# Kernel optimization log

Hardware: AMD Instinct MI355X
Metric: run time of the kernel (lower is better)

The kernel has to match this reference:

```python
import jax, jax.numpy as jnp
import numpy as np

IRREPS = [(32, 0), (16, 1), (8, 2)]          # (multiplicity, l)
DIMS = [m * (2 * l + 1) for m, l in IRREPS]  # [32, 48, 40]
OFF = np.concatenate([[0], np.cumsum(DIMS)]).astype(int)
FEAT = int(OFF[-1])                          # 120
H = 4                                        # num_heads
EPS = 1e-5
N_NODES = 50000
N_EDGES = 800000


def split(x):
    # split last axis into per-irrep blocks [..., mul, 2l+1]
    return [x[..., OFF[i]:OFF[i + 1]].reshape(x.shape[:-1] + (m, 2 * l + 1))
            for i, (m, l) in enumerate(IRREPS)]


def merge(blocks, lead):
    return jnp.concatenate([b.reshape(lead + (-1,)) for b in blocks], axis=-1)


def o3_linear(x, Ws):
    # e3nn o3.Linear: mixes multiplicities within each irrep type, 1/sqrt(fan_in) norm
    bs = split(x)
    out = [jnp.einsum('...im,io->...om', b, W) / np.sqrt(m)
           for b, W, (m, l) in zip(bs, Ws, IRREPS)]
    return merge(out, x.shape[:-1])


def norm_act(x):
    # e3nn nn.NormActivation with sigmoid: y = sigmoid(|x|) * x / |x| per irrep
    out = []
    for b in split(x):
        n = jnp.sqrt(jnp.sum(b * b, axis=-1, keepdims=True) + EPS * EPS)
        out.append(jax.nn.sigmoid(n) * b / n)
    return merge(out, x.shape[:-1])


def tp_dot(q, k, Wd):
    # FullyConnectedTensorProduct(q_ir, k_ir, 'Hx0e'), component normalization:
    # per-edge weighted inner products between matching irreps -> [E, H]
    fan = sum(m * m * (2 * l + 1) for m, l in IRREPS)
    out = 0.0
    for qb, kb, W, (m, l) in zip(split(q), split(k), Wd, IRREPS):
        out = out + jnp.einsum('eim,ejm,ijh->eh', qb, kb, W) / np.sqrt(2 * l + 1)
    return out / np.sqrt(fan)


def setup_inputs() -> dict:
    key = jax.random.key(0)
    ks = jax.random.split(key, 16)
    inp = {"node_features": jax.random.normal(ks[0], (N_NODES, FEAT), jnp.float32)}
    i = 1
    for name in ("Wq", "Wk", "Wv"):
        for j, (m, l) in enumerate(IRREPS):
            inp[f"{name}{j}"] = jax.random.normal(ks[i], (m, m), jnp.float32); i += 1
    for j, (m, l) in enumerate(IRREPS):
        inp[f"Wd{j}"] = jax.random.normal(ks[i], (m, m, H), jnp.float32); i += 1
    inp["edge_dst"] = jax.random.randint(ks[i], (N_EDGES,), 0, N_NODES); i += 1
    inp["edge_src"] = jax.random.randint(ks[i], (N_EDGES,), 0, N_NODES)
    return inp


def reference(node_features, Wq0, Wq1, Wq2, Wk0, Wk1, Wk2, Wv0, Wv1, Wv2,
              Wd0, Wd1, Wd2, edge_dst, edge_src):
    N = node_features.shape[0]
    q = norm_act(o3_linear(node_features, [Wq0, Wq1, Wq2]))              # [N, F]
    k = norm_act(o3_linear(node_features[edge_src], [Wk0, Wk1, Wk2]))    # [E, F]
    v_node = norm_act(o3_linear(node_features, [Wv0, Wv1, Wv2]))         # [N, F]
    v = v_node[edge_src]                                                 # [E, F]
    exp = jnp.exp(tp_dot(q[edge_dst], k, [Wd0, Wd1, Wd2]))               # [E, H]
    exp = jnp.mean(exp, axis=1, keepdims=True)                           # [E, 1]
    z = jax.ops.segment_sum(exp, edge_dst, num_segments=N)               # [N, 1]
    z = jnp.where(z == 0, 1.0, z)
    alpha = exp / z[edge_dst]                                            # [E, 1]
    f_out = jax.ops.segment_sum(jnp.sqrt(jax.nn.relu(alpha)) * v,
                                edge_dst, num_segments=N)                # [N, F]
    return f_out + v_node
```

## Files before the change

### kernel.cpp

```cpp
#include <hip/hip_runtime.h>
#include <math.h>

#define FEAT 120
#define HCNT 4

typedef unsigned short ushort_t;
typedef unsigned int uint_t;
typedef __attribute__((ext_vector_type(8))) short short8;
typedef __attribute__((ext_vector_type(4))) float floatx4;

__device__ __forceinline__ float nact_scale(float sumsq) {
    float n = sqrtf(sumsq + 1e-10f);
    float sig = 1.0f / (1.0f + expf(-n));
    return sig / n;
}

__device__ __forceinline__ ushort_t bf16r(float f) {
    uint_t u = __float_as_uint(f);
    u += 0x7fff + ((u >> 16) & 1);
    return (ushort_t)(u >> 16);
}

#define INV_S32 0.17677669529663687f
#define INV_S16 0.25f
#define INV_S8  0.35355339059327373f
#define S_IR0 0.02175970668223486f
#define S_IR1 0.012562972567021898f
#define S_IR2 0.009731317442393031f


__global__ __launch_bounds__(256) void zero_int_kernel(int* __restrict__ p, int n) {
    int i = blockIdx.x * 256 + threadIdx.x;
    if (i < n) p[i] = 0;
}

__global__ __launch_bounds__(256) void hist_kernel(const int* __restrict__ dst,
                                                   int* __restrict__ cnt, int E) {
    int e = blockIdx.x * 256 + threadIdx.x;
    if (e < E) atomicAdd(&cnt[dst[e]], 1);
}

__global__ __launch_bounds__(256) void scan_block_kernel(const int* __restrict__ cnt,
                                                         int* __restrict__ excl,
                                                         int* __restrict__ bsum, int n) {
    __shared__ int s[256];
    int t = threadIdx.x;
    int i = blockIdx.x * 256 + t;
    int v = (i < n) ? cnt[i] : 0;
    s[t] = v;
    __syncthreads();
    for (int off = 1; off < 256; off <<= 1) {
        int add = (t >= off) ? s[t - off] : 0;
        __syncthreads();
        s[t] += add;
        __syncthreads();
    }
    if (i < n) excl[i] = s[t] - v;
    if (t == 255) bsum[blockIdx.x] = s[255];
}

__global__ __launch_bounds__(256) void scan_sums_kernel(int* __restrict__ bsum, int nb) {
    __shared__ int s[256];
    int t = threadIdx.x;
    int v = (t < nb) ? bsum[t] : 0;
    s[t] = v;
    __syncthreads();
    for (int off = 1; off < 256; off <<= 1) {
        int add = (t >= off) ? s[t - off] : 0;
        __syncthreads();
        s[t] += add;
        __syncthreads();
    }
    if (t < nb) bsum[t] = s[t] - v;
}

__global__ __launch_bounds__(256) void add_offsets_kernel(int* __restrict__ offsets,
                                                          const int* __restrict__ bsum,
                                                          int* __restrict__ cursor,
                                                          int n, int E) {
    int i = blockIdx.x * 256 + threadIdx.x;
    if (i < n) {
        int off = offsets[i] + bsum[i >> 8];
        offsets[i] = off;
        cursor[i] = off;
    }
    if (i == 0) offsets[n] = E;
}

__global__ __launch_bounds__(256) void scatter_kernel(const int* __restrict__ dst,
                                                      const int* __restrict__ src,
                                                      int* __restrict__ cursor,
                                                      int* __restrict__ ssrc, int E) {
    int e = blockIdx.x * 256 + threadIdx.x;
    if (e < E) {
        int pos = atomicAdd(&cursor[dst[e]], 1);
        ssrc[pos] = src[e];
    }
}


__global__ __launch_bounds__(256) void node_qkv_kernel(
    const float* __restrict__ x,
    const float* __restrict__ Wq0, const float* __restrict__ Wq1, const float* __restrict__ Wq2,
    const float* __restrict__ Wk0, const float* __restrict__ Wk1, const float* __restrict__ Wk2,
    const float* __restrict__ Wv0, const float* __restrict__ Wv1, const float* __restrict__ Wv2,
    float* __restrict__ qnode, ushort_t* __restrict__ kb, ushort_t* __restrict__ vb,
    float* __restrict__ out, int N)
{
    __shared__ float sWq0[1024], sWq1[256], sWq2[64];
    __shared__ float sWk0[1024], sWk1[256], sWk2[64];
    __shared__ float sWv0[1024], sWv1[256], sWv2[64];

    int t = threadIdx.x;
    for (int i = t; i < 1024; i += 256) { sWq0[i] = Wq0[i]; sWk0[i] = Wk0[i]; sWv0[i] = Wv0[i]; }
    if (t < 256) { sWq1[t] = Wq1[t]; sWk1[t] = Wk1[t]; sWv1[t] = Wv1[t]; }
    if (t < 64)  { sWq2[t] = Wq2[t]; sWk2[t] = Wk2[t]; sWv2[t] = Wv2[t]; }
    __syncthreads();

    int lane = t & 63, wid = t >> 6;
    int ngrp = (N + 3) >> 2;
    for (int grp = blockIdx.x; grp < ngrp; grp += gridDim.x) {
        int node = __builtin_amdgcn_readfirstlane(grp * 4 + wid);
        if (node >= N) continue;
        const float* xr = x + (size_t)node * FEAT;
        float* qr = qnode + (size_t)node * FEAT;
        ushort_t* kr = kb + (size_t)node * 128;
        ushort_t* vr = vb + (size_t)node * 128;
        float* orow = out + (size_t)node * FEAT;
        if (lane < 32) {
            int o = lane;
            float q = 0, k = 0, v = 0;
            #pragma unroll 8
            for (int i = 0; i < 32; i++) {
                float xi = xr[i];
                q = fmaf(xi, sWq0[i * 32 + o], q);
                k = fmaf(xi, sWk0[i * 32 + o], k);
                v = fmaf(xi, sWv0[i * 32 + o], v);
            }
            q *= INV_S32; k *= INV_S32; v *= INV_S32;
            q *= nact_scale(q * q);
            k *= nact_scale(k * k);
            v *= nact_scale(v * v);
            qr[o] = q; kr[o] = bf16r(k); vr[o] = bf16r(v); orow[o] = v;
        } else if (lane < 48) {
            int o = lane - 32;
            float q[3] = {0,0,0}, k[3] = {0,0,0}, v[3] = {0,0,0};
            for (int i = 0; i < 16; i++) {
                float wq = sWq1[i * 16 + o], wk = sWk1[i * 16 + o], wv = sWv1[i * 16 + o];
                #pragma unroll
                for (int c = 0; c < 3; c++) {
                    float xi = xr[32 + i * 3 + c];
                    q[c] = fmaf(xi, wq, q[c]);
                    k[c] = fmaf(xi, wk, k[c]);
                    v[c] = fmaf(xi, wv, v[c]);
                }
            }
            float nq = 0, nk = 0, nv = 0;
            #pragma unroll
            for (int c = 0; c < 3; c++) {
                q[c] *= INV_S16; k[c] *= INV_S16; v[c] *= INV_S16;
                nq += q[c]*q[c]; nk += k[c]*k[c]; nv += v[c]*v[c];
            }
            float sq = nact_scale(nq), sk = nact_scale(nk), sv = nact_scale(nv);
            #pragma unroll
            for (int c = 0; c < 3; c++) {
                int f = 32 + o * 3 + c;
                float vv = v[c]*sv;
                qr[f] = q[c]*sq; kr[f] = bf16r(k[c]*sk); vr[f] = bf16r(vv); orow[f] = vv;
            }
        } else if (lane < 56) {
            int o = lane - 48;
            float q[5] = {0,0,0,0,0}, k[5] = {0,0,0,0,0}, v[5] = {0,0,0,0,0};
            for (int i = 0; i < 8; i++) {
                float wq = sWq2[i * 8 + o], wk = sWk2[i * 8 + o], wv = sWv2[i * 8 + o];
                #pragma unroll
                for (int c = 0; c < 5; c++) {
                    float xi = xr[80 + i * 5 + c];
                    q[c] = fmaf(xi, wq, q[c]);
                    k[c] = fmaf(xi, wk, k[c]);
                    v[c] = fmaf(xi, wv, v[c]);
                }
            }
            float nq = 0, nk = 0, nv = 0;
            #pragma unroll
            for (int c = 0; c < 5; c++) {
                q[c] *= INV_S8; k[c] *= INV_S8; v[c] *= INV_S8;
                nq += q[c]*q[c]; nk += k[c]*k[c]; nv += v[c]*v[c];
            }
            float sq = nact_scale(nq), sk = nact_scale(nk), sv = nact_scale(nv);
            #pragma unroll
            for (int c = 0; c < 5; c++) {
                int f = 80 + o * 5 + c;
                float vv = v[c]*sv;
                qr[f] = q[c]*sq; kr[f] = bf16r(k[c]*sk); vr[f] = bf16r(vv); orow[f] = vv;
            }
        } else {
            int p = 120 + (lane - 56);
            kr[p] = 0; vr[p] = 0;
        }
    }
}


__global__ __launch_bounds__(256) void node_tq_kernel(
    const float* __restrict__ qnode,
    const float* __restrict__ Wd0, const float* __restrict__ Wd1, const float* __restrict__ Wd2,
    ushort_t* __restrict__ tqb, int N)
{
    __shared__ float4 sWd0[1024];
    __shared__ float4 sWd1[256];
    __shared__ float4 sWd2[64];
    __shared__ float qs[4][FEAT];

    int t = threadIdx.x;
    for (int i = t; i < 1024; i += 256) sWd0[i] = ((const float4*)Wd0)[i];
    if (t < 256) sWd1[t] = ((const float4*)Wd1)[t];
    if (t < 64)  sWd2[t] = ((const float4*)Wd2)[t];
    __syncthreads();

    int lane = t & 63, wid = t >> 6;
    int ngrp = (N + 3) >> 2;
    for (int grp = blockIdx.x; grp < ngrp; grp += gridDim.x) {
        int node = __builtin_amdgcn_readfirstlane(grp * 4 + wid);
        if (node >= N) continue;
        const float* qr = qnode + (size_t)node * FEAT;
        qs[wid][lane] = qr[lane];
        if (lane < FEAT - 64) qs[wid][64 + lane] = qr[64 + lane];
        __builtin_amdgcn_wave_barrier();

        ushort_t* tr = tqb + (size_t)node * 512;
        if (lane < 32) {
            int j = lane;
            float a0 = 0, a1 = 0, a2 = 0, a3 = 0;
            #pragma unroll 8
            for (int i = 0; i < 32; i++) {
                float qi = qs[wid][i];
                float4 w = sWd0[i * 32 + j];
                a0 = fmaf(qi, w.x, a0); a1 = fmaf(qi, w.y, a1);
                a2 = fmaf(qi, w.z, a2); a3 = fmaf(qi, w.w, a3);
            }
            tr[0 * 128 + j] = bf16r(a0 * S_IR0);
            tr[1 * 128 + j] = bf16r(a1 * S_IR0);
            tr[2 * 128 + j] = bf16r(a2 * S_IR0);
            tr[3 * 128 + j] = bf16r(a3 * S_IR0);
        } else if (lane < 48) {
            int j = lane - 32;
            float a[4][3] = {};
            for (int i = 0; i < 16; i++) {
                float4 w = sWd1[i * 16 + j];
                #pragma unroll
                for (int c = 0; c < 3; c++) {
                    float qi = qs[wid][32 + i * 3 + c];
                    a[0][c] = fmaf(qi, w.x, a[0][c]);
                    a[1][c] = fmaf(qi, w.y, a[1][c]);
                    a[2][c] = fmaf(qi, w.z, a[2][c]);
                    a[3][c] = fmaf(qi, w.w, a[3][c]);
                }
            }
            #pragma unroll
            for (int h = 0; h < 4; h++)
                #pragma unroll
                for (int c = 0; c < 3; c++)
                    tr[h * 128 + 32 + j * 3 + c] = bf16r(a[h][c] * S_IR1);
        } else if (lane < 56) {
            int j = lane - 48;
            float a[4][5] = {};
            for (int i = 0; i < 8; i++) {
                float4 w = sWd2[i * 8 + j];
                #pragma unroll
                for (int c = 0; c < 5; c++) {
                    float qi = qs[wid][80 + i * 5 + c];
                    a[0][c] = fmaf(qi, w.x, a[0][c]);
                    a[1][c] = fmaf(qi, w.y, a[1][c]);
                    a[2][c] = fmaf(qi, w.z, a[2][c]);
                    a[3][c] = fmaf(qi, w.w, a[3][c]);
                }
            }
            #pragma unroll
            for (int h = 0; h < 4; h++)
                #pragma unroll
                for (int c = 0; c < 5; c++)
                    tr[h * 128 + 80 + j * 5 + c] = bf16r(a[h][c] * S_IR2);
        } else {
            int r = lane - 56;
            #pragma unroll
            for (int h = 0; h < 4; h++) tr[h * 128 + 120 + r] = 0;
        }
        __builtin_amdgcn_wave_barrier();
    }
}


__global__ __launch_bounds__(256) void edge_mfma_kernel(
    const ushort_t* __restrict__ tqb, const ushort_t* __restrict__ kb,
    const ushort_t* __restrict__ vb,
    const int* __restrict__ offsets, const int* __restrict__ ssrc,
    float* __restrict__ out, int N)
{
    int lane = threadIdx.x & 63, wid = threadIdx.x >> 6;
    int node = blockIdx.x * 4 + wid;
    if (node >= N) return;
    node = __builtin_amdgcn_readfirstlane(node);
    int m = lane & 15, quad = lane >> 4;

    short8 afr[4];
    if (m < HCNT) {
        const short8* ap = (const short8*)(tqb + (size_t)node * 512 + m * 128 + quad * 8);
        #pragma unroll
        for (int b = 0; b < 4; b++) afr[b] = ap[b * 4];
    } else {
        #pragma unroll
        for (int b = 0; b < 4; b++) afr[b] = (short8){0,0,0,0,0,0,0,0};
    }

    int beg = offsets[node], end = offsets[node + 1];
    float zpart = 0.0f, accx = 0.0f, accy = 0.0f;
    const uint_t* vrow = (const uint_t*)vb;

    for (int tb = beg; tb < end; tb += 16) {
        int rem = end - tb; if (rem > 16) rem = 16;
        int idx = tb + (m < rem ? m : rem - 1);
        int src = ssrc[idx];
        const short8* bp = (const short8*)(kb + (size_t)src * 128 + quad * 8);
        short8 b0 = bp[0], b1 = bp[4], b2 = bp[8], b3 = bp[12];
        floatx4 C = {0.0f, 0.0f, 0.0f, 0.0f};
        C = __builtin_amdgcn_mfma_f32_16x16x32_bf16(afr[0], b0, C, 0, 0, 0);
        C = __builtin_amdgcn_mfma_f32_16x16x32_bf16(afr[1], b1, C, 0, 0, 0);
        C = __builtin_amdgcn_mfma_f32_16x16x32_bf16(afr[2], b2, C, 0, 0, 0);
        C = __builtin_amdgcn_mfma_f32_16x16x32_bf16(afr[3], b3, C, 0, 0, 0);

        float w = 0.0f;
        if (quad == 0 && m < rem) {
            float ex = 0.25f * (__expf(C[0]) + __expf(C[1]) + __expf(C[2]) + __expf(C[3]));
            zpart += ex;
            w = sqrtf(ex);
        }

        if (rem == 16) {
            #pragma unroll
            for (int e0 = 0; e0 < 16; e0 += 8) {
                float we[8]; int se[8]; uint_t vp[8];
                #pragma unroll
                for (int j = 0; j < 8; j++) {
                    we[j] = __shfl(w, e0 + j, 64);
                    se[j] = __shfl(src, e0 + j, 64);
                }
                #pragma unroll
                for (int j = 0; j < 8; j++) vp[j] = vrow[(size_t)se[j] * 64 + lane];
                #pragma unroll
                for (int j = 0; j < 8; j++) {
                    accx = fmaf(we[j], __uint_as_float(vp[j] << 16), accx);
                    accy = fmaf(we[j], __uint_as_float(vp[j] & 0xffff0000u), accy);
                }
            }
        } else {
            for (int e = 0; e < rem; e++) {
                float we = __shfl(w, e, 64);
                int   se = __shfl(src, e, 64);
                uint_t vp = vrow[(size_t)se * 64 + lane];
                accx = fmaf(we, __uint_as_float(vp << 16), accx);
                accy = fmaf(we, __uint_as_float(vp & 0xffff0000u), accy);
            }
        }
    }

    zpart += __shfl_xor(zpart, 1, 64);
    zpart += __shfl_xor(zpart, 2, 64);
    zpart += __shfl_xor(zpart, 4, 64);
    zpart += __shfl_xor(zpart, 8, 64);
    float zsum = __shfl(zpart, 0, 64);
    float scale = (zsum > 0.0f) ? rsqrtf(zsum) : 0.0f;

    if (lane < 60) {
        float2* op = (float2*)(out + (size_t)node * FEAT) + lane;
        float2 o = *op;
        o.x = fmaf(accx, scale, o.x);
        o.y = fmaf(accy, scale, o.y);
        *op = o;
    }
}


extern "C" void kernel_launch(void* const* d_in, const int* in_sizes, int n_in,
                              void* d_out, int out_size, void* d_ws, size_t ws_size,
                              hipStream_t stream) {
    const float* x   = (const float*)d_in[0];
    const float* Wq0 = (const float*)d_in[1];
    const float* Wq1 = (const float*)d_in[2];
    const float* Wq2 = (const float*)d_in[3];
    const float* Wk0 = (const float*)d_in[4];
    const float* Wk1 = (const float*)d_in[5];
    const float* Wk2 = (const float*)d_in[6];
    const float* Wv0 = (const float*)d_in[7];
    const float* Wv1 = (const float*)d_in[8];
    const float* Wv2 = (const float*)d_in[9];
    const float* Wd0 = (const float*)d_in[10];
    const float* Wd1 = (const float*)d_in[11];
    const float* Wd2 = (const float*)d_in[12];
    const int* edge_dst = (const int*)d_in[13];
    const int* edge_src = (const int*)d_in[14];
    float* out = (float*)d_out;

    int N = in_sizes[0] / FEAT;
    int E = in_sizes[13];

    float* ws = (float*)d_ws;
    float* qnode = ws;
    ushort_t* kb  = (ushort_t*)(qnode + (size_t)N * FEAT);
    ushort_t* vb  = kb + (size_t)N * 128;
    ushort_t* tqb = vb + (size_t)N * 128;
    int* offsets = (int*)(tqb + (size_t)N * 512);
    int* cursor  = offsets + (N + 1);
    int* bsum    = cursor + N;
    int* ssrc    = bsum + 256;

    int NB = (N + 255) / 256;
    int EB = (E + 255) / 256;
    int NW = (N + 3) / 4;

    zero_int_kernel<<<NB, 256, 0, stream>>>(cursor, N);
    hist_kernel<<<EB, 256, 0, stream>>>(edge_dst, cursor, E);
    scan_block_kernel<<<NB, 256, 0, stream>>>(cursor, offsets, bsum, N);
    scan_sums_kernel<<<1, 256, 0, stream>>>(bsum, NB);
    add_offsets_kernel<<<NB, 256, 0, stream>>>(offsets, bsum, cursor, N, E);
    scatter_kernel<<<EB, 256, 0, stream>>>(edge_dst, edge_src, cursor, ssrc, E);

    node_qkv_kernel<<<2048, 256, 0, stream>>>(x, Wq0, Wq1, Wq2, Wk0, Wk1, Wk2,
                                              Wv0, Wv1, Wv2, qnode, kb, vb, out, N);
    node_tq_kernel<<<2048, 256, 0, stream>>>(qnode, Wd0, Wd1, Wd2, tqb, N);
    edge_mfma_kernel<<<NW, 256, 0, stream>>>(tqb, kb, vb, offsets, ssrc, out, N);
}
```

Measured before the change: 398.7 us.

## Rewrite node projections: thread-per-node QKV, MFMA-based Wd transform, bf16 q

Precomputes transposed, pre-scaled projection weights and a zero-padded block-diagonal bf16 Wd matrix in small prep kernels. The QKV projection becomes one thread per node per projection, with weights read uniformly from global memory. The q-times-Wd transform becomes a 16x16x32 bf16 MFMA GEMM over 16-node tiles. q is now stored in bf16, and the residual v is re-read from the bf16 buffer in the edge kernel instead of being written to out early. This is meant to cut node-stage ALU and LDS costs and fp32 q traffic. The trade-offs are extra bf16 precision loss, higher register pressure from 120-float per-thread arrays, and added small launches.

```diff
diff --git a/kernel.cpp b/kernel.cpp
--- a/kernel.cpp
+++ b/kernel.cpp
@@ -99,194 +99,160 @@
 }
 
 
-__global__ __launch_bounds__(256) void node_qkv_kernel(
-    const float* __restrict__ x,
+__global__ __launch_bounds__(256) void prep_zero_kernel(uint_t* __restrict__ p, int nwords) {
+    int i = blockIdx.x * 256 + threadIdx.x;
+    if (i < nwords) p[i] = 0;
+}
+
+__global__ __launch_bounds__(256) void prep_fill_kernel(
     const float* __restrict__ Wq0, const float* __restrict__ Wq1, const float* __restrict__ Wq2,
     const float* __restrict__ Wk0, const float* __restrict__ Wk1, const float* __restrict__ Wk2,
     const float* __restrict__ Wv0, const float* __restrict__ Wv1, const float* __restrict__ Wv2,
-    float* __restrict__ qnode, ushort_t* __restrict__ kb, ushort_t* __restrict__ vb,
-    float* __restrict__ out, int N)
+    const float* __restrict__ Wd0, const float* __restrict__ Wd1, const float* __restrict__ Wd2,
+    float* __restrict__ wt, ushort_t* __restrict__ wdtb)
 {
-    __shared__ float sWq0[1024], sWq1[256], sWq2[64];
-    __shared__ float sWk0[1024], sWk1[256], sWk2[64];
-    __shared__ float sWv0[1024], sWv1[256], sWv2[64];
-
     int t = threadIdx.x;
-    for (int i = t; i < 1024; i += 256) { sWq0[i] = Wq0[i]; sWk0[i] = Wk0[i]; sWv0[i] = Wv0[i]; }
-    if (t < 256) { sWq1[t] = Wq1[t]; sWk1[t] = Wk1[t]; sWv1[t] = Wv1[t]; }
-    if (t < 64)  { sWq2[t] = Wq2[t]; sWk2[t] = Wk2[t]; sWv2[t] = Wv2[t]; }
-    __syncthreads();
-
-    int lane = t & 63, wid = t >> 6;
-    int ngrp = (N + 3) >> 2;
-    for (int grp = blockIdx.x; grp < ngrp; grp += gridDim.x) {
-        int node = __builtin_amdgcn_readfirstlane(grp * 4 + wid);
-        if (node >= N) continue;
-        const float* xr = x + (size_t)node * FEAT;
-        float* qr = qnode + (size_t)node * FEAT;
-        ushort_t* kr = kb + (size_t)node * 128;
-        ushort_t* vr = vb + (size_t)node * 128;
-        float* orow = out + (size_t)node * FEAT;
-        if (lane < 32) {
-            int o = lane;
-            float q = 0, k = 0, v = 0;
-            #pragma unroll 8
-            for (int i = 0; i < 32; i++) {
-                float xi = xr[i];
-                q = fmaf(xi, sWq0[i * 32 + o], q);
-                k = fmaf(xi, sWk0[i * 32 + o], k);
-                v = fmaf(xi, sWv0[i * 32 + o], v);
-            }
-            q *= INV_S32; k *= INV_S32; v *= INV_S32;
-            q *= nact_scale(q * q);
-            k *= nact_scale(k * k);
-            v *= nact_scale(v * v);
-            qr[o] = q; kr[o] = bf16r(k); vr[o] = bf16r(v); orow[o] = v;
-        } else if (lane < 48) {
-            int o = lane - 32;
-            float q[3] = {0,0,0}, k[3] = {0,0,0}, v[3] = {0,0,0};
-            for (int i = 0; i < 16; i++) {
-                float wq = sWq1[i * 16 + o], wk = sWk1[i * 16 + o], wv = sWv1[i * 16 + o];
-                #pragma unroll
-                for (int c = 0; c < 3; c++) {
-                    float xi = xr[32 + i * 3 + c];
-                    q[c] = fmaf(xi, wq, q[c]);
-                    k[c] = fmaf(xi, wk, k[c]);
-                    v[c] = fmaf(xi, wv, v[c]);
-                }
-            }
-            float nq = 0, nk = 0, nv = 0;
-            #pragma unroll
-            for (int c = 0; c < 3; c++) {
-                q[c] *= INV_S16; k[c] *= INV_S16; v[c] *= INV_S16;
-                nq += q[c]*q[c]; nk += k[c]*k[c]; nv += v[c]*v[c];
-            }
-            float sq = nact_scale(nq), sk = nact_scale(nk), sv = nact_scale(nv);
-            #pragma unroll
-            for (int c = 0; c < 3; c++) {
-                int f = 32 + o * 3 + c;
-                float vv = v[c]*sv;
-                qr[f] = q[c]*sq; kr[f] = bf16r(k[c]*sk); vr[f] = bf16r(vv); orow[f] = vv;
-            }
-        } else if (lane < 56) {
-            int o = lane - 48;
-            float q[5] = {0,0,0,0,0}, k[5] = {0,0,0,0,0}, v[5] = {0,0,0,0,0};
-            for (int i = 0; i < 8; i++) {
-                float wq = sWq2[i * 8 + o], wk = sWk2[i * 8 + o], wv = sWv2[i * 8 + o];
-                #pragma unroll
-                for (int c = 0; c < 5; c++) {
-                    float xi = xr[80 + i * 5 + c];
-                    q[c] = fmaf(xi, wq, q[c]);
-                    k[c] = fmaf(xi, wk, k[c]);
-                    v[c] = fmaf(xi, wv, v[c]);
-                }
-            }
-            float nq = 0, nk = 0, nv = 0;
-            #pragma unroll
-            for (int c = 0; c < 5; c++) {
-                q[c] *= INV_S8; k[c] *= INV_S8; v[c] *= INV_S8;
-                nq += q[c]*q[c]; nk += k[c]*k[c]; nv += v[c]*v[c];
-            }
-            float sq = nact_scale(nq), sk = nact_scale(nk), sv = nact_scale(nv);
-            #pragma unroll
-            for (int c = 0; c < 5; c++) {
-                int f = 80 + o * 5 + c;
-                float vv = v[c]*sv;
-                qr[f] = q[c]*sq; kr[f] = bf16r(k[c]*sk); vr[f] = bf16r(vv); orow[f] = vv;
-            }
-        } else {
-            int p = 120 + (lane - 56);
-            kr[p] = 0; vr[p] = 0;
-        }
-    }
-}
-
-
-__global__ __launch_bounds__(256) void node_tq_kernel(
-    const float* __restrict__ qnode,
-    const float* __restrict__ Wd0, const float* __restrict__ Wd1, const float* __restrict__ Wd2,
+    for (int it = t; it < 3072; it += 256) {
+        int p = it >> 10, rem = it & 1023, o = rem >> 5, i = rem & 31;
+        const float* W = (p == 0) ? Wq0 : (p == 1) ? Wk0 : Wv0;
+        wt[p * 1344 + o * 32 + i] = W[i * 32 + o] * INV_S32;
+    }
+    for (int it = t; it < 768; it += 256) {
+        int p = it >> 8, rem = it & 255, o = rem >> 4, i = rem & 15;
+        const float* W = (p == 0) ? Wq1 : (p == 1) ? Wk1 : Wv1;
+        wt[p * 1344 + 1024 + o * 16 + i] = W[i * 16 + o] * INV_S16;
+    }
+    for (int it = t; it < 192; it += 256) {
+        int p = it / 64, rem = it % 64, o = rem >> 3, i = rem & 7;
+        const float* W = (p == 0) ? Wq2 : (p == 1) ? Wk2 : Wv2;
+        wt[p * 1344 + 1280 + o * 8 + i] = W[i * 8 + o] * INV_S8;
+    }
+    for (int it = t; it < 4096; it += 256) {
+        int i = it / 128, rem = it % 128, j = rem / 4, h = rem % 4;
+        wdtb[(h * 128 + j) * 128 + i] = bf16r(Wd0[i * 128 + j * 4 + h] * S_IR0);
+    }
+    for (int it = t; it < 3072; it += 256) {
+        int i = it / 192, rem = it % 192, j = rem / 12, r2 = rem % 12, c = r2 / 4, h = r2 % 4;
+        wdtb[(h * 128 + 32 + j * 3 + c) * 128 + (32 + i * 3 + c)] = bf16r(Wd1[i * 64 + j * 4 + h] * S_IR1);
+    }
+    for (int it = t; it < 1280; it += 256) {
+        int i = it / 160, rem = it % 160, j = rem / 20, r2 = rem % 20, c = r2 / 4, h = r2 % 4;
+        wdtb[(h * 128 + 80 + j * 5 + c) * 128 + (80 + i * 5 + c)] = bf16r(Wd2[i * 32 + j * 4 + h] * S_IR2);
+    }
+}
+
+
+#define EMIT(f, val) do { \
+    if ((f) & 1) yp[(f) >> 1] = (uint_t)bf16r(prev) | ((uint_t)bf16r(val) << 16); \
+    else prev = (val); } while (0)
+
+__global__ __launch_bounds__(256) void node_qkv_v2_kernel(
+    const float* __restrict__ x, const float* __restrict__ wt,
+    ushort_t* __restrict__ qb, ushort_t* __restrict__ kb, ushort_t* __restrict__ vb, int N)
+{
+    int node = blockIdx.x * 256 + threadIdx.x;
+    int p = blockIdx.y;
+    if (node >= N) return;
+
+    float xr[FEAT];
+    const float4* xp = (const float4*)(x + (size_t)node * FEAT);
+    #pragma unroll
+    for (int i = 0; i < 30; i++) ((float4*)xr)[i] = xp[i];
+
+    const float* W = wt + p * 1344;
+    uint_t yp[64];
+    float prev = 0.0f;
+
+    #pragma unroll
+    for (int o = 0; o < 32; o++) {
+        float acc = 0.0f;
+        const float* w0 = W + o * 32;
+        #pragma unroll
+        for (int i = 0; i < 32; i++) acc = fmaf(w0[i], xr[i], acc);
+        float y = acc * nact_scale(acc * acc);
+        EMIT(o, y);
+    }
+    #pragma unroll
+    for (int o = 0; o < 16; o++) {
+        float a0 = 0.0f, a1 = 0.0f, a2 = 0.0f;
+        const float* w1 = W + 1024 + o * 16;
+        #pragma unroll
+        for (int i = 0; i < 16; i++) {
+            float w = w1[i];
+            a0 = fmaf(w, xr[32 + i * 3 + 0], a0);
+            a1 = fmaf(w, xr[32 + i * 3 + 1], a1);
+            a2 = fmaf(w, xr[32 + i * 3 + 2], a2);
+        }
+        float s = nact_scale(a0 * a0 + a1 * a1 + a2 * a2);
+        EMIT(32 + o * 3 + 0, a0 * s);
+        EMIT(32 + o * 3 + 1, a1 * s);
+        EMIT(32 + o * 3 + 2, a2 * s);
+    }
+    #pragma unroll
+    for (int o = 0; o < 8; o++) {
+        float a0 = 0.0f, a1 = 0.0f, a2 = 0.0f, a3 = 0.0f, a4 = 0.0f;
+        const float* w2 = W + 1280 + o * 8;
+        #pragma unroll
+        for (int i = 0; i < 8; i++) {
+            float w = w2[i];
+            a0 = fmaf(w, xr[80 + i * 5 + 0], a0);
+            a1 = fmaf(w, xr[80 + i * 5 + 1], a1);
+            a2 = fmaf(w, xr[80 + i * 5 + 2], a2);
+            a3 = fmaf(w, xr[80 + i * 5 + 3], a3);
+            a4 = fmaf(w, xr[80 + i * 5 + 4], a4);
+        }
+        float s = nact_scale(a0*a0 + a1*a1 + a2*a2 + a3*a3 + a4*a4);
+        EMIT(80 + o * 5 + 0, a0 * s);
+        EMIT(80 + o * 5 + 1, a1 * s);
+        EMIT(80 + o * 5 + 2, a2 * s);
+        EMIT(80 + o * 5 + 3, a3 * s);
+        EMIT(80 + o * 5 + 4, a4 * s);
+    }
+    yp[60] = 0; yp[61] = 0; yp[62] = 0; yp[63] = 0;
+
+    ushort_t* dstp = (p == 0) ? qb : (p == 1) ? kb : vb;
+    uint4* dst = (uint4*)(dstp + (size_t)node * 128);
+    #pragma unroll
+    for (int i = 0; i < 16; i++) {
+        uint4 v4;
+        v4.x = yp[4*i]; v4.y = yp[4*i+1]; v4.z = yp[4*i+2]; v4.w = yp[4*i+3];
+        dst[i] = v4;
+    }
+}
+#undef EMIT
+
+
+__global__ __launch_bounds__(256, 2) void node_tq_mfma_kernel(
+    const ushort_t* __restrict__ qb, const ushort_t* __restrict__ wdtb,
     ushort_t* __restrict__ tqb, int N)
 {
-    __shared__ float4 sWd0[1024];
-    __shared__ float4 sWd1[256];
-    __shared__ float4 sWd2[64];
-    __shared__ float qs[4][FEAT];
-
-    int t = threadIdx.x;
-    for (int i = t; i < 1024; i += 256) sWd0[i] = ((const float4*)Wd0)[i];
-    if (t < 256) sWd1[t] = ((const float4*)Wd1)[t];
-    if (t < 64)  sWd2[t] = ((const float4*)Wd2)[t];
-    __syncthreads();
-
-    int lane = t & 63, wid = t >> 6;
-    int ngrp = (N + 3) >> 2;
-    for (int grp = blockIdx.x; grp < ngrp; grp += gridDim.x) {
-        int node = __builtin_amdgcn_readfirstlane(grp * 4 + wid);
-        if (node >= N) continue;
-        const float* qr = qnode + (size_t)node * FEAT;
-        qs[wid][lane] = qr[lane];
-        if (lane < FEAT - 64) qs[wid][64 + lane] = qr[64 + lane];
-        __builtin_amdgcn_wave_barrier();
-
-        ushort_t* tr = tqb + (size_t)node * 512;
-        if (lane < 32) {
-            int j = lane;
-            float a0 = 0, a1 = 0, a2 = 0, a3 = 0;
-            #pragma unroll 8
-            for (int i = 0; i < 32; i++) {
-                float qi = qs[wid][i];
-                float4 w = sWd0[i * 32 + j];
-                a0 = fmaf(qi, w.x, a0); a1 = fmaf(qi, w.y, a1);
-                a2 = fmaf(qi, w.z, a2); a3 = fmaf(qi, w.w, a3);
-            }
-            tr[0 * 128 + j] = bf16r(a0 * S_IR0);
-            tr[1 * 128 + j] = bf16r(a1 * S_IR0);
-            tr[2 * 128 + j] = bf16r(a2 * S_IR0);
-            tr[3 * 128 + j] = bf16r(a3 * S_IR0);
-        } else if (lane < 48) {
-            int j = lane - 32;
-            float a[4][3] = {};
-            for (int i = 0; i < 16; i++) {
-                float4 w = sWd1[i * 16 + j];
-                #pragma unroll
-                for (int c = 0; c < 3; c++) {
-                    float qi = qs[wid][32 + i * 3 + c];
-                    a[0][c] = fmaf(qi, w.x, a[0][c]);
-                    a[1][c] = fmaf(qi, w.y, a[1][c]);
-                    a[2][c] = fmaf(qi, w.z, a[2][c]);
-                    a[3][c] = fmaf(qi, w.w, a[3][c]);
-                }
-            }
-            #pragma unroll
-            for (int h = 0; h < 4; h++)
-                #pragma unroll
-                for (int c = 0; c < 3; c++)
-                    tr[h * 128 + 32 + j * 3 + c] = bf16r(a[h][c] * S_IR1);
-        } else if (lane < 56) {
-            int j = lane - 48;
-            float a[4][5] = {};
-            for (int i = 0; i < 8; i++) {
-                float4 w = sWd2[i * 8 + j];
-                #pragma unroll
-                for (int c = 0; c < 5; c++) {
-                    float qi = qs[wid][80 + i * 5 + c];
-                    a[0][c] = fmaf(qi, w.x, a[0][c]);
-                    a[1][c] = fmaf(qi, w.y, a[1][c]);
-                    a[2][c] = fmaf(qi, w.z, a[2][c]);
-                    a[3][c] = fmaf(qi, w.w, a[3][c]);
-                }
-            }
-            #pragma unroll
-            for (int h = 0; h < 4; h++)
-                #pragma unroll
-                for (int c = 0; c < 5; c++)
-                    tr[h * 128 + 80 + j * 5 + c] = bf16r(a[h][c] * S_IR2);
-        } else {
-            int r = lane - 56;
-            #pragma unroll
-            for (int h = 0; h < 4; h++) tr[h * 128 + 120 + r] = 0;
-        }
-        __builtin_amdgcn_wave_barrier();
+    int t = threadIdx.x, lane = t & 63, w = t >> 6;
+    int base = blockIdx.x * 16;
+    int nl = lane & 15, quad = lane >> 4;
+    int node = base + nl;
+    int nclamp = (node < N) ? node : (N - 1);
+
+    short8 bfr[4];
+    const ushort_t* bp = qb + (size_t)nclamp * 128 + quad * 8;
+    #pragma unroll
+    for (int kk = 0; kk < 4; kk++) bfr[kk] = *(const short8*)(bp + kk * 32);
+
+    #pragma unroll
+    for (int ti = 0; ti < 8; ti++) {
+        int tile = w * 8 + ti;
+        const ushort_t* ap = wdtb + (tile * 16 + nl) * 128 + quad * 8;
+        floatx4 C = {0.0f, 0.0f, 0.0f, 0.0f};
+        #pragma unroll
+        for (int kk = 0; kk < 4; kk++) {
+            short8 a = *(const short8*)(ap + kk * 32);
+            C = __builtin_amdgcn_mfma_f32_16x16x32_bf16(a, bfr[kk], C, 0, 0, 0);
+        }
+        if (node < N) {
+            uint_t lo = (uint_t)bf16r(C[0]) | ((uint_t)bf16r(C[1]) << 16);
+            uint_t hi = (uint_t)bf16r(C[2]) | ((uint_t)bf16r(C[3]) << 16);
+            uint_t* dst = (uint_t*)(tqb + (size_t)node * 512 + tile * 16 + quad * 4);
+            dst[0] = lo; dst[1] = hi;
+        }
     }
 }
 
@@ -372,11 +338,11 @@
     float scale = (zsum > 0.0f) ? rsqrtf(zsum) : 0.0f;
 
     if (lane < 60) {
-        float2* op = (float2*)(out + (size_t)node * FEAT) + lane;
-        float2 o = *op;
-        o.x = fmaf(accx, scale, o.x);
-        o.y = fmaf(accy, scale, o.y);
-        *op = o;
+        uint_t vself = vrow[(size_t)node * 64 + lane];
+        float2 o;
+        o.x = fmaf(accx, scale, __uint_as_float(vself << 16));
+        o.y = fmaf(accy, scale, __uint_as_float(vself & 0xffff0000u));
+        *((float2*)(out + (size_t)node * FEAT) + lane) = o;
     }
 }
 
@@ -404,12 +370,13 @@
     int N = in_sizes[0] / FEAT;
     int E = in_sizes[13];
 
-    float* ws = (float*)d_ws;
-    float* qnode = ws;
-    ushort_t* kb  = (ushort_t*)(qnode + (size_t)N * FEAT);
-    ushort_t* vb  = kb + (size_t)N * 128;
-    ushort_t* tqb = vb + (size_t)N * 128;
-    int* offsets = (int*)(tqb + (size_t)N * 512);
+    ushort_t* kb   = (ushort_t*)d_ws;
+    ushort_t* vb   = kb + (size_t)N * 128;
+    ushort_t* qb   = vb + (size_t)N * 128;
+    ushort_t* tqb  = qb + (size_t)N * 128;
+    ushort_t* wdtb = tqb + (size_t)N * 512;
+    float* wt      = (float*)(wdtb + 65536);
+    int* offsets = (int*)(wt + 4032);
     int* cursor  = offsets + (N + 1);
     int* bsum    = cursor + N;
     int* ssrc    = bsum + 256;
@@ -417,6 +384,11 @@
     int NB = (N + 255) / 256;
     int EB = (E + 255) / 256;
     int NW = (N + 3) / 4;
+    int NT = (N + 15) / 16;
+
+    prep_zero_kernel<<<128, 256, 0, stream>>>((uint_t*)wdtb, 32768);
+    prep_fill_kernel<<<1, 256, 0, stream>>>(Wq0, Wq1, Wq2, Wk0, Wk1, Wk2,
+                                            Wv0, Wv1, Wv2, Wd0, Wd1, Wd2, wt, wdtb);
 
     zero_int_kernel<<<NB, 256, 0, stream>>>(cursor, N);
     hist_kernel<<<EB, 256, 0, stream>>>(edge_dst, cursor, E);
@@ -425,8 +397,7 @@
     add_offsets_kernel<<<NB, 256, 0, stream>>>(offsets, bsum, cursor, N, E);
     scatter_kernel<<<EB, 256, 0, stream>>>(edge_dst, edge_src, cursor, ssrc, E);
 
-    node_qkv_kernel<<<2048, 256, 0, stream>>>(x, Wq0, Wq1, Wq2, Wk0, Wk1, Wk2,
-                                              Wv0, Wv1, Wv2, qnode, kb, vb, out, N);
-    node_tq_kernel<<<2048, 256, 0, stream>>>(qnode, Wd0, Wd1, Wd2, tqb, N);
+    node_qkv_v2_kernel<<<dim3(NB, 3), 256, 0, stream>>>(x, wt, qb, kb, vb, N);
+    node_tq_mfma_kernel<<<NT, 256, 0, stream>>>(qb, wdtb, tqb, N);
     edge_mfma_kernel<<<NW, 256, 0, stream>>>(tqb, kb, vb, offsets, ssrc, out, N);
 }
```

Result: slower. 417.6 us (+4.7%).
